# Optimization experiments

Hardware: AMD Instinct MI355X
Metric: run time of the kernel (lower is better)

## Reference

```python
import jax, jax.numpy as jnp
import numpy as np

B, T, D, SPAN = 4, 4096, 1024, 128


def _windowed_attention(q, k, v, span):
    # Causal sliding-window attention: position t attends to [max(0, t-span+1), t].
    # Tiled as blocks of size span: each query block attends to its own block
    # plus the previous block (exactly covers the window), avoiding any [T,T]
    # or per-timestep materialization.
    B, T, D = q.shape
    S = span
    nb = T // S  # T chosen divisible by span
    qb = q.reshape(B, nb, S, D)
    kb = k.reshape(B, nb, S, D)
    vb = v.reshape(B, nb, S, D)
    pad = jnp.zeros((B, 1, S, D), dtype=q.dtype)
    kk = jnp.concatenate([jnp.concatenate([pad, kb[:, :-1]], axis=1), kb], axis=2)  # [B,nb,2S,D]
    vv = jnp.concatenate([jnp.concatenate([pad, vb[:, :-1]], axis=1), vb], axis=2)  # [B,nb,2S,D]
    scale = 1.0 / jnp.sqrt(jnp.asarray(D, dtype=q.dtype))
    scores = jnp.einsum('bnqd,bnkd->bnqk', qb, kk) * scale  # [B,nb,S,2S]
    n_idx = jnp.arange(nb)[:, None, None]      # block index
    q_idx = jnp.arange(S)[None, :, None]       # query offset within block
    k_idx = jnp.arange(2 * S)[None, None, :]   # key offset in [prev|cur] pair
    rel = k_idx - S - q_idx                    # key_pos - query_pos
    # window: -span+1 <= rel <= 0; first block's "previous" half is padding -> mask it
    mask = (rel <= 0) & (rel > -S) & ((n_idx > 0) | (k_idx >= S))
    neg = jnp.asarray(jnp.finfo(scores.dtype).min, dtype=scores.dtype)
    scores = jnp.where(mask, scores, neg)
    w = jax.nn.softmax(scores, axis=-1)
    out = jnp.einsum('bnqk,bnkd->bnqd', w, vv)
    return out.reshape(B, T, D)


def setup_inputs() -> dict:
    key = jax.random.key(0)
    ks = jax.random.split(key, 7)
    s = 1.0 / np.sqrt(D)
    return {
        'x': jax.random.normal(ks[0], (B, T, D), dtype=jnp.float32),
        'Wq': jax.random.normal(ks[1], (D, D), dtype=jnp.float32) * s,
        'bq': jax.random.normal(ks[2], (D,), dtype=jnp.float32) * s,
        'Wk': jax.random.normal(ks[3], (D, D), dtype=jnp.float32) * s,
        'bk': jax.random.normal(ks[4], (D,), dtype=jnp.float32) * s,
        'Wv': jax.random.normal(ks[5], (D, D), dtype=jnp.float32) * s,
        'bv': jax.random.normal(ks[6], (D,), dtype=jnp.float32) * s,
        'span': SPAN,
    }


def reference(x, Wq, bq, Wk, bk, Wv, bv, span):
    # torch nn.Linear: y = x @ W.T + b
    q = jnp.einsum('btd,ed->bte', x, Wq) + bq
    k = jnp.einsum('btd,ed->bte', x, Wk) + bk
    v = jnp.einsum('btd,ed->bte', x, Wv) + bv
    return _windowed_attention(q, k, v, span)
```

## Files before the change

kernel.cpp:

```cpp
#include <hip/hip_runtime.h>
#include <hip/hip_bf16.h>

#define BB 4
#define TT 4096
#define DD 1024
#define SS 128
#define MM (BB*TT)

typedef __attribute__((ext_vector_type(8))) short bf16x8;
typedef __attribute__((ext_vector_type(4))) short s16x4;
typedef __attribute__((ext_vector_type(4))) float f32x4;

#define VMCNT(N) asm volatile("s_waitcnt vmcnt(" #N ")" ::: "memory")
#define LGKM0()  asm volatile("s_waitcnt lgkmcnt(0)" ::: "memory")

__device__ __forceinline__ void block_sync() {
    asm volatile("" ::: "memory");
    __builtin_amdgcn_s_barrier();
    asm volatile("" ::: "memory");
}

__device__ __forceinline__ short f2bf(float f) {
    union { float f; unsigned u; } cv; cv.f = f;
    unsigned u = cv.u;
    u += 0x7fffu + ((u >> 16) & 1u);
    return (short)(u >> 16);
}

__device__ __forceinline__ void gload16(const short* g, short* l) {
    __builtin_amdgcn_global_load_lds(
        (const __attribute__((address_space(1))) void*)g,
        (__attribute__((address_space(3))) void*)l, 16, 0, 0);
}

__global__ __launch_bounds__(256) void cast_f32_bf16(
    const float* __restrict__ src, short* __restrict__ dst)
{
    const int i = (blockIdx.x * 256 + threadIdx.x) * 4;
    const float4 v = *(const float4*)(src + i);
    s16x4 o;
    o.x = f2bf(v.x); o.y = f2bf(v.y); o.z = f2bf(v.z); o.w = f2bf(v.w);
    *(s16x4*)(dst + i) = o;
}

__global__ __launch_bounds__(256) void cast_w3(
    const float* __restrict__ a, const float* __restrict__ b,
    const float* __restrict__ c, short* __restrict__ dst)
{
    const float* src = (blockIdx.y == 0) ? a : (blockIdx.y == 1) ? b : c;
    short* d = dst + (size_t)blockIdx.y * DD * DD;
    const int i = (blockIdx.x * 256 + threadIdx.x) * 4;
    const float4 v = *(const float4*)(src + i);
    s16x4 o;
    o.x = f2bf(v.x); o.y = f2bf(v.y); o.z = f2bf(v.z); o.w = f2bf(v.w);
    *(s16x4*)(d + i) = o;
}


#define MF(a_, b_, c_) ((GRP == 2)                                            \
    ? __builtin_amdgcn_mfma_f32_16x16x32_bf16((b_), (a_), (c_), 0, 0, 0)      \
    : __builtin_amdgcn_mfma_f32_16x16x32_bf16((a_), (b_), (c_), 0, 0, 0))

#define QKV_PHASE(ABASE, P, STAGE_STMT, VM_STMT)                              \
  do {                                                                        \
    bf16x8 af0k0 = *(const bf16x8*)((ABASE) + (((P)*2)*16   + c16) * 64 + sw0);\
    bf16x8 af0k1 = *(const bf16x8*)((ABASE) + (((P)*2)*16   + c16) * 64 + sw1);\
    bf16x8 af1k0 = *(const bf16x8*)((ABASE) + (((P)*2+1)*16 + c16) * 64 + sw0);\
    bf16x8 af1k1 = *(const bf16x8*)((ABASE) + (((P)*2+1)*16 + c16) * 64 + sw1);\
    STAGE_STMT;                                                               \
    block_sync();                                                             \
    LGKM0();                                                                  \
    __builtin_amdgcn_s_setprio(1);                                            \
    _Pragma("unroll")                                                         \
    for (int nj = 0; nj < 4; nj++) {                                          \
      acc[(P)*2][nj]   = MF(af0k0, bf[nj][0], acc[(P)*2][nj]);                \
      acc[(P)*2][nj]   = MF(af0k1, bf[nj][1], acc[(P)*2][nj]);                \
      acc[(P)*2+1][nj] = MF(af1k0, bf[nj][0], acc[(P)*2+1][nj]);              \
      acc[(P)*2+1][nj] = MF(af1k1, bf[nj][1], acc[(P)*2+1][nj]);              \
    }                                                                         \
    __builtin_amdgcn_s_setprio(0);                                            \
    VM_STMT;                                                                  \
    block_sync();                                                             \
  } while (0)

template<int GRP>
__device__ __forceinline__ void qkv_core(
    const short* __restrict__ X, const short* __restrict__ W,
    const float* __restrict__ bias,
    short* __restrict__ Y, short* __restrict__ vT,
    short* lds, const int m_base, const int n_base)
{
    const int tid  = threadIdx.x;
    const int wv   = tid >> 6, lane = tid & 63;
    const int wm   = wv >> 2,  wn   = wv & 3;
    const int quad = lane >> 4, c16 = lane & 15;
    const int swz  = c16 & 7;
    const int sw0  = ((quad)     ^ swz) * 8;
    const int sw1  = ((quad + 4) ^ swz) * 8;

    auto stageA = [&](int k0, int d, int h) {
        short* dst = lds + d * 16384 + h * 8192;
#pragma unroll
        for (int g = 0; g < 2; g++) {
            const int idx = g * 512 + tid;
            const int row = idx >> 3, slot = idx & 7;
            gload16(X + (size_t)(m_base + h * 128 + row) * DD + k0
                      + ((slot ^ (row & 7)) * 8),
                    dst + row * 64 + slot * 8);
        }
    };
    auto stageB = [&](int k0, int d, int h) {
        short* dst = lds + 32768 + d * 16384 + h * 8192;
#pragma unroll
        for (int g = 0; g < 2; g++) {
            const int idx = g * 512 + tid;
            const int row = idx >> 3, slot = idx & 7;
            gload16(W + (size_t)(n_base + h * 128 + row) * DD + k0
                      + ((slot ^ (row & 7)) * 8),
                    dst + row * 64 + slot * 8);
        }
    };

    f32x4 acc[8][4];
#pragma unroll
    for (int i = 0; i < 8; i++)
#pragma unroll
        for (int j = 0; j < 4; j++) acc[i][j] = (f32x4){0.f, 0.f, 0.f, 0.f};

    stageA(0, 0, 0);  stageA(0, 0, 1);
    stageB(0, 0, 0);  stageB(0, 0, 1);
    stageB(64, 1, 0); stageB(64, 1, 1);
    VMCNT(4);
    block_sync();

    const short* Abuf0 = lds + wm * 8192;
    const short* Abuf1 = lds + 16384 + wm * 8192;
    const short* Bbuf0 = lds + 32768 + (wn >> 1) * 8192 + (wn & 1) * 4096;
    const short* Bbuf1 = lds + 49152 + (wn >> 1) * 8192 + (wn & 1) * 4096;

    bf16x8 bf[4][2];

    for (int it = 0; it < 8; ++it) {
        const int k1 = it * 128 + 64;
        const int k2 = it * 128 + 128;
        const int k3 = it * 128 + 192;
        const bool more = (it < 7);

#pragma unroll
        for (int nj = 0; nj < 4; nj++) {
            bf[nj][0] = *(const bf16x8*)(Bbuf0 + (nj * 16 + c16) * 64 + sw0);
            bf[nj][1] = *(const bf16x8*)(Bbuf0 + (nj * 16 + c16) * 64 + sw1);
        }
        QKV_PHASE(Abuf0, 0, stageA(k1, 1, 0), ((void)0));
        QKV_PHASE(Abuf0, 1, stageA(k1, 1, 1), ((void)0));
        QKV_PHASE(Abuf0, 2, if (more) stageB(k2, 0, 0), ((void)0));
        QKV_PHASE(Abuf0, 3, if (more) stageB(k2, 0, 1),
                  if (more) { VMCNT(4); } else { VMCNT(0); });

#pragma unroll
        for (int nj = 0; nj < 4; nj++) {
            bf[nj][0] = *(const bf16x8*)(Bbuf1 + (nj * 16 + c16) * 64 + sw0);
            bf[nj][1] = *(const bf16x8*)(Bbuf1 + (nj * 16 + c16) * 64 + sw1);
        }
        QKV_PHASE(Abuf1, 0, if (more) stageA(k2, 0, 0), ((void)0));
        QKV_PHASE(Abuf1, 1, if (more) stageA(k2, 0, 1), ((void)0));
        QKV_PHASE(Abuf1, 2, if (more) stageB(k3, 1, 0), ((void)0));
        QKV_PHASE(Abuf1, 3, if (more) stageB(k3, 1, 1),
                  if (more) { VMCNT(4); } else { VMCNT(0); });
    }

    if (GRP != 2) {
#pragma unroll
        for (int nj = 0; nj < 4; nj++) {
            const int col = n_base + wn * 64 + nj * 16 + c16;
            const float bc = bias[col];
#pragma unroll
            for (int mi = 0; mi < 8; mi++) {
                const int row = m_base + wm * 128 + mi * 16 + quad * 4;
#pragma unroll
                for (int r = 0; r < 4; r++)
                    Y[(size_t)(row + r) * DD + col] = f2bf(acc[mi][nj][r] + bc);
            }
        }
    } else {
#pragma unroll
        for (int nj = 0; nj < 4; nj++) {
#pragma unroll
            for (int r = 0; r < 4; r++) {
                const int drow = n_base + wn * 64 + nj * 16 + quad * 4 + r;
                const float bc = bias[drow];
#pragma unroll
                for (int mi = 0; mi < 8; mi++) {
                    const int mcol = m_base + wm * 128 + mi * 16 + c16;
                    vT[((size_t)(mcol >> 12) * DD + drow) * TT + (mcol & 4095)]
                        = f2bf(acc[mi][nj][r] + bc);
                }
            }
        }
    }
}

__global__ __launch_bounds__(512, 2) void qkv_gemm8(
    const short* __restrict__ X, const short* __restrict__ W3,
    const float* __restrict__ bq, const float* __restrict__ bk,
    const float* __restrict__ bv,
    short* __restrict__ q, short* __restrict__ k, short* __restrict__ vT)
{
    __shared__ __align__(16) short lds[65536];
    const int bid = blockIdx.x;
    const int wg  = (bid & 7) * 96 + (bid >> 3);
    const int mt  = wg & 63;
    const int cn  = wg >> 6;
    const int grp = cn >> 2;
    const int nt  = cn & 3;
    const int m_base = mt * 256;
    const int n_base = nt * 256;
    if (grp == 0)      qkv_core<0>(X, W3,              bq, q, nullptr, lds, m_base, n_base);
    else if (grp == 1) qkv_core<1>(X, W3 + DD * DD,    bk, k, nullptr, lds, m_base, n_base);
    else               qkv_core<2>(X, W3 + 2 * DD * DD, bv, nullptr, vT, lds, m_base, n_base);
}

__global__ __launch_bounds__(256) void attn_fused(
    const short* __restrict__ Q,
    const short* __restrict__ Kb,
    const short* __restrict__ VT,
    float* __restrict__ O)
{
    __shared__ short lds[78336];

    const int l   = blockIdx.x;
    const int xcd = l & 7;
    const int rr  = l >> 3;
    const int n   = xcd * 4 + (rr & 3);
    const int qh  = (rr >> 2) & 1;
    const int b   = rr >> 3;

    const int tid  = threadIdx.x;
    const int wv   = tid >> 6, lane = tid & 63;
    const int quad = lane >> 4, c16 = lane & 15;
    const int srow = tid >> 2;
    const int scol = (tid & 3) * 8;

    const int qrow   = b * TT + n * SS + qh * 64;
    const int krow   = b * TT + n * SS - SS;
    const int bstart = b * TT;

    f32x4 acc[16];
#pragma unroll
    for (int j = 0; j < 16; j++) acc[j] = (f32x4){0.f, 0.f, 0.f, 0.f};

    auto stage1 = [&](int kk, int bi) {
        short* qb   = lds + bi * 20480;
        short* kbuf = qb + 4096;
        const int k0 = kk * 64;
#pragma unroll
        for (int ks = 0; ks < 2; ks++) {
            gload16(Q + (qrow + srow) * DD + k0 + ks * 32 + scol,
                    qb + ks * 2048 + srow * 32 + scol);
#pragma unroll
            for (int s = 0; s < 4; s++) {
                const int row = srow + s * 64;
                int g = krow + row;
                if (g < bstart) g = bstart;
                gload16(Kb + g * DD + k0 + ks * 32 + scol,
                        kbuf + ks * 8192 + row * 32 + scol);
            }
        }
    };

    stage1(0, 0);
    stage1(1, 1);
    for (int kk = 0; kk < 16; kk++) {
        if (kk < 15) { VMCNT(10); } else { VMCNT(0); }
        block_sync();
        if (kk < 14) stage1(kk + 2, (kk + 2) % 3);
        const short* qb   = lds + (kk % 3) * 20480;
        const short* kbuf = qb + 4096;
#pragma unroll
        for (int ks = 0; ks < 2; ks++) {
            bf16x8 a = *(const bf16x8*)(qb + ks * 2048 + (wv * 16 + c16) * 32 + quad * 8);
#pragma unroll
            for (int j = 0; j < 16; j++) {
                bf16x8 bf = *(const bf16x8*)(kbuf + ks * 8192 + (j * 16 + c16) * 32 + quad * 8);
                acc[j] = __builtin_amdgcn_mfma_f32_16x16x32_bf16(a, bf, acc[j], 0, 0, 0);
            }
        }
    }

    __syncthreads();

    const int tbase = n * SS - SS;
    auto stage2 = [&](int s, short* vbuf) {
        const int d0 = (s >> 1) * 128;
        const int kh = (s & 1) * 128;
#pragma unroll
        for (int kc = 0; kc < 4; kc++) {
#pragma unroll
            for (int s64 = 0; s64 < 2; s64++) {
                const int row = srow + s64 * 64;
                int t = tbase + kh + kc * 32 + scol;
                if (t < 0) t = 0;
                gload16(VT + (size_t)(b * DD + d0 + row) * TT + t,
                        vbuf + kc * 4096 + row * 32 + scol);
            }
        }
    };
    stage2(0, lds);
    stage2(1, lds + 16384);

    short* Pw = lds + 61440 + wv * (16 * 264);
    const float scale = 0.03125f;
#pragma unroll
    for (int r = 0; r < 4; r++) {
        const int q_idx = qh * 64 + wv * 16 + quad * 4 + r;
        float mx = -3.0e38f;
#pragma unroll
        for (int j = 0; j < 16; j++) {
            const int k_idx = j * 16 + c16;
            const int rel = k_idx - SS - q_idx;
            const bool valid = (rel <= 0) & (rel > -SS) & ((n > 0) | (k_idx >= SS));
            const float sv = valid ? acc[j][r] * scale : -3.0e38f;
            acc[j][r] = sv;
            mx = fmaxf(mx, sv);
        }
#pragma unroll
        for (int o = 1; o < 16; o <<= 1) mx = fmaxf(mx, __shfl_xor(mx, o));
        float sm = 0.f;
#pragma unroll
        for (int j = 0; j < 16; j++) {
            const float p = __expf(acc[j][r] - mx);
            acc[j][r] = p;
            sm += p;
        }
#pragma unroll
        for (int o = 1; o < 16; o <<= 1) sm += __shfl_xor(sm, o);
        const float inv = 1.0f / sm;
#pragma unroll
        for (int j = 0; j < 16; j++)
            Pw[(quad * 4 + r) * 264 + j * 16 + c16] = f2bf(acc[j][r] * inv);
    }

    f32x4 o8[8];
#pragma unroll
    for (int j = 0; j < 8; j++) o8[j] = (f32x4){0.f, 0.f, 0.f, 0.f};

    for (int s = 0; s < 16; s++) {
        if (s < 2)       { VMCNT(8); }
        else if (s < 15) { VMCNT(40); }
        else             { VMCNT(16); }
        block_sync();
        if (s < 14) stage2(s + 2, lds + ((s + 2) % 3) * 16384);
        const short* vbuf = lds + (s % 3) * 16384;
        const int kh = (s & 1) * 128;
#pragma unroll
        for (int kc = 0; kc < 4; kc++) {
            bf16x8 a = *(const bf16x8*)(Pw + c16 * 264 + kh + kc * 32 + quad * 8);
#pragma unroll
            for (int jj = 0; jj < 8; jj++) {
                bf16x8 bf = *(const bf16x8*)(vbuf + kc * 4096 + (jj * 16 + c16) * 32 + quad * 8);
                o8[jj] = __builtin_amdgcn_mfma_f32_16x16x32_bf16(a, bf, o8[jj], 0, 0, 0);
            }
        }
        if (s & 1) {
            const int d0 = (s >> 1) * 128;
#pragma unroll
            for (int jj = 0; jj < 8; jj++) {
#pragma unroll
                for (int r = 0; r < 4; r++)
                    O[(size_t)(qrow + wv * 16 + quad * 4 + r) * DD + d0 + jj * 16 + c16] = o8[jj][r];
                o8[jj] = (f32x4){0.f, 0.f, 0.f, 0.f};
            }
        }
    }
}

extern "C" void kernel_launch(void* const* d_in, const int* in_sizes, int n_in,
                              void* d_out, int out_size, void* d_ws, size_t ws_size,
                              hipStream_t stream) {
    const float* x  = (const float*)d_in[0];
    const float* Wq = (const float*)d_in[1];
    const float* bq = (const float*)d_in[2];
    const float* Wk = (const float*)d_in[3];
    const float* bk = (const float*)d_in[4];
    const float* Wv = (const float*)d_in[5];
    const float* bv = (const float*)d_in[6];
    float* out = (float*)d_out;

    char* ws = (char*)d_ws;
    const size_t SZ = (size_t)MM * DD * 2;
    short* q   = (short*)(ws);
    short* k   = (short*)(ws + SZ);
    short* vT  = (short*)(ws + 2 * SZ);
    short* xb  = (short*)(ws + 3 * SZ);
    short* w3b = (short*)(ws + 4 * SZ);

    dim3 blk(256);
    cast_f32_bf16<<<MM * DD / 1024, blk, 0, stream>>>(x, xb);
    cast_w3<<<dim3(DD * DD / 1024, 3), blk, 0, stream>>>(Wq, Wk, Wv, w3b);

    qkv_gemm8<<<768, 512, 0, stream>>>(xb, w3b, bq, bk, bv, q, k, vT);

    attn_fused<<<256, 256, 0, stream>>>(q, k, vT, out);
}
```

Baseline: 300.2 us.

## Split attention across 8 waves with key-half softmax reduction and swizzled LDS

The attention kernel now launches 512 threads instead of 256. Each pair of waves splits the 256 keys (for QK^T) or the 64-wide head dimension chunks (for PV), and row max and sum are combined across the pair through LDS with extra barriers. Q/K and V tiles use XOR-swizzled LDS layouts to cut bank conflicts, and s_setprio is raised around the MFMA loops. All outputs are held in 32 accumulator registers and written once at the end, which raises register pressure against the 512-thread, 2-block launch bound.

```diff
diff --git a/kernel.cpp b/kernel.cpp
--- a/kernel.cpp
+++ b/kernel.cpp
@@ -220,7 +220,7 @@
     else               qkv_core<2>(X, W3 + 2 * DD * DD, bv, nullptr, vT, lds, m_base, n_base);
 }
 
-__global__ __launch_bounds__(256) void attn_fused(
+__global__ __launch_bounds__(512, 2) void attn_fused(
     const short* __restrict__ Q,
     const short* __restrict__ Kb,
     const short* __restrict__ VT,
@@ -238,85 +238,95 @@
     const int tid  = threadIdx.x;
     const int wv   = tid >> 6, lane = tid & 63;
     const int quad = lane >> 4, c16 = lane & 15;
-    const int srow = tid >> 2;
-    const int scol = (tid & 3) * 8;
+    const int qt   = wv >> 1;
+    const int kh   = wv & 1;
+    const int dh   = wv & 1;
 
     const int qrow   = b * TT + n * SS + qh * 64;
     const int krow   = b * TT + n * SS - SS;
     const int bstart = b * TT;
 
-    f32x4 acc[16];
-#pragma unroll
-    for (int j = 0; j < 16; j++) acc[j] = (f32x4){0.f, 0.f, 0.f, 0.f};
+    f32x4 acc[8];
+#pragma unroll
+    for (int j = 0; j < 8; j++) acc[j] = (f32x4){0.f, 0.f, 0.f, 0.f};
 
     auto stage1 = [&](int kk, int bi) {
-        short* qb   = lds + bi * 20480;
-        short* kbuf = qb + 4096;
+        short* qb = lds + bi * 20480;
+        short* kb = qb + 4096;
         const int k0 = kk * 64;
-#pragma unroll
-        for (int ks = 0; ks < 2; ks++) {
-            gload16(Q + (qrow + srow) * DD + k0 + ks * 32 + scol,
-                    qb + ks * 2048 + srow * 32 + scol);
-#pragma unroll
-            for (int s = 0; s < 4; s++) {
-                const int row = srow + s * 64;
-                int g = krow + row;
-                if (g < bstart) g = bstart;
-                gload16(Kb + g * DD + k0 + ks * 32 + scol,
-                        kbuf + ks * 8192 + row * 32 + scol);
-            }
+        {
+            const int row = tid >> 3, slot = tid & 7;
+            gload16(Q + (qrow + row) * DD + k0 + ((slot ^ (row & 7)) * 8),
+                    qb + row * 64 + slot * 8);
+        }
+#pragma unroll
+        for (int g = 0; g < 4; g++) {
+            const int idx = g * 512 + tid;
+            const int row = idx >> 3, slot = idx & 7;
+            int grow = krow + row;
+            if (grow < bstart) grow = bstart;
+            gload16(Kb + grow * DD + k0 + ((slot ^ (row & 7)) * 8),
+                    kb + row * 64 + slot * 8);
         }
     };
+
+    const int sw7 = c16 & 7;
 
     stage1(0, 0);
     stage1(1, 1);
     for (int kk = 0; kk < 16; kk++) {
-        if (kk < 15) { VMCNT(10); } else { VMCNT(0); }
+        if (kk < 15) { VMCNT(5); } else { VMCNT(0); }
         block_sync();
         if (kk < 14) stage1(kk + 2, (kk + 2) % 3);
-        const short* qb   = lds + (kk % 3) * 20480;
-        const short* kbuf = qb + 4096;
+        const short* qb = lds + (kk % 3) * 20480;
+        const short* kb = qb + 4096;
+        __builtin_amdgcn_s_setprio(1);
 #pragma unroll
         for (int ks = 0; ks < 2; ks++) {
-            bf16x8 a = *(const bf16x8*)(qb + ks * 2048 + (wv * 16 + c16) * 32 + quad * 8);
-#pragma unroll
-            for (int j = 0; j < 16; j++) {
-                bf16x8 bf = *(const bf16x8*)(kbuf + ks * 8192 + (j * 16 + c16) * 32 + quad * 8);
+            const int slot = ((ks * 4 + quad) ^ sw7) * 8;
+            bf16x8 a = *(const bf16x8*)(qb + (qt * 16 + c16) * 64 + slot);
+#pragma unroll
+            for (int j = 0; j < 8; j++) {
+                bf16x8 bf = *(const bf16x8*)(kb + (kh * 128 + j * 16 + c16) * 64 + slot);
                 acc[j] = __builtin_amdgcn_mfma_f32_16x16x32_bf16(a, bf, acc[j], 0, 0, 0);
             }
         }
-    }
-
-    __syncthreads();
+        __builtin_amdgcn_s_setprio(0);
+    }
+
+    block_sync();
 
     const int tbase = n * SS - SS;
-    auto stage2 = [&](int s, short* vbuf) {
-        const int d0 = (s >> 1) * 128;
-        const int kh = (s & 1) * 128;
-#pragma unroll
-        for (int kc = 0; kc < 4; kc++) {
-#pragma unroll
-            for (int s64 = 0; s64 < 2; s64++) {
-                const int row = srow + s64 * 64;
-                int t = tbase + kh + kc * 32 + scol;
-                if (t < 0) t = 0;
-                gload16(VT + (size_t)(b * DD + d0 + row) * TT + t,
-                        vbuf + kc * 4096 + row * 32 + scol);
-            }
+    auto stage2 = [&](int s, int bi) {
+        short* vb = lds + bi * 16384;
+        const int d0  = (s >> 1) * 128;
+        const int khv = (s & 1) * 128;
+#pragma unroll
+        for (int g = 0; g < 4; g++) {
+            const int idx = g * 512 + tid;
+            const int row = idx >> 4, slot = idx & 15;
+            int t = tbase + khv + ((slot ^ (row & 15)) * 8);
+            if (t < 0) t = 0;
+            gload16(VT + (size_t)(b * DD + d0 + row) * TT + t,
+                    vb + row * 128 + slot * 8);
         }
     };
-    stage2(0, lds);
-    stage2(1, lds + 16384);
-
-    short* Pw = lds + 61440 + wv * (16 * 264);
+    stage2(0, 0);
+    stage2(1, 1);
+
+    short* Pb   = lds + 61440;
+    float* smax = (float*)(lds + 49152);
+    float* ssum = (float*)(lds + 49408);
     const float scale = 0.03125f;
+    float mx4[4], sums[4];
+
 #pragma unroll
     for (int r = 0; r < 4; r++) {
-        const int q_idx = qh * 64 + wv * 16 + quad * 4 + r;
+        const int q_idx = qh * 64 + qt * 16 + quad * 4 + r;
         float mx = -3.0e38f;
 #pragma unroll
-        for (int j = 0; j < 16; j++) {
-            const int k_idx = j * 16 + c16;
+        for (int j = 0; j < 8; j++) {
+            const int k_idx = kh * 128 + j * 16 + c16;
             const int rel = k_idx - SS - q_idx;
             const bool valid = (rel <= 0) & (rel > -SS) & ((n > 0) | (k_idx >= SS));
             const float sv = valid ? acc[j][r] * scale : -3.0e38f;
@@ -325,53 +335,71 @@
         }
 #pragma unroll
         for (int o = 1; o < 16; o <<= 1) mx = fmaxf(mx, __shfl_xor(mx, o));
+        mx4[r] = mx;
+        if (c16 == 0) smax[(qt * 2 + kh) * 16 + quad * 4 + r] = mx;
+    }
+    LGKM0(); block_sync();
+
+#pragma unroll
+    for (int r = 0; r < 4; r++) {
+        const float M = fmaxf(mx4[r], smax[(qt * 2 + (kh ^ 1)) * 16 + quad * 4 + r]);
         float sm = 0.f;
 #pragma unroll
-        for (int j = 0; j < 16; j++) {
-            const float p = __expf(acc[j][r] - mx);
+        for (int j = 0; j < 8; j++) {
+            const float p = __expf(acc[j][r] - M);
             acc[j][r] = p;
             sm += p;
         }
 #pragma unroll
         for (int o = 1; o < 16; o <<= 1) sm += __shfl_xor(sm, o);
-        const float inv = 1.0f / sm;
-#pragma unroll
-        for (int j = 0; j < 16; j++)
-            Pw[(quad * 4 + r) * 264 + j * 16 + c16] = f2bf(acc[j][r] * inv);
-    }
-
-    f32x4 o8[8];
-#pragma unroll
-    for (int j = 0; j < 8; j++) o8[j] = (f32x4){0.f, 0.f, 0.f, 0.f};
-
+        sums[r] = sm;
+        if (c16 == 0) ssum[(qt * 2 + kh) * 16 + quad * 4 + r] = sm;
+    }
+    LGKM0(); block_sync();
+
+#pragma unroll
+    for (int r = 0; r < 4; r++) {
+        const float inv = 1.0f / (sums[r] + ssum[(qt * 2 + (kh ^ 1)) * 16 + quad * 4 + r]);
+#pragma unroll
+        for (int j = 0; j < 8; j++)
+            Pb[(qt * 16 + quad * 4 + r) * 264 + kh * 128 + j * 16 + c16] = f2bf(acc[j][r] * inv);
+    }
+    LGKM0();
+
+    f32x4 o_all[32];
+#pragma unroll
+    for (int j = 0; j < 32; j++) o_all[j] = (f32x4){0.f, 0.f, 0.f, 0.f};
+
+#pragma unroll
     for (int s = 0; s < 16; s++) {
-        if (s < 2)       { VMCNT(8); }
-        else if (s < 15) { VMCNT(40); }
-        else             { VMCNT(16); }
+        if (s < 15) { VMCNT(4); } else { VMCNT(0); }
         block_sync();
-        if (s < 14) stage2(s + 2, lds + ((s + 2) % 3) * 16384);
-        const short* vbuf = lds + (s % 3) * 16384;
-        const int kh = (s & 1) * 128;
+        if (s < 14) stage2(s + 2, (s + 2) % 3);
+        const short* vb = lds + (s % 3) * 16384;
+        const int khP = (s & 1) * 128;
+        const int od  = (s >> 1) * 4;
+        __builtin_amdgcn_s_setprio(1);
 #pragma unroll
         for (int kc = 0; kc < 4; kc++) {
-            bf16x8 a = *(const bf16x8*)(Pw + c16 * 264 + kh + kc * 32 + quad * 8);
-#pragma unroll
-            for (int jj = 0; jj < 8; jj++) {
-                bf16x8 bf = *(const bf16x8*)(vbuf + kc * 4096 + (jj * 16 + c16) * 32 + quad * 8);
-                o8[jj] = __builtin_amdgcn_mfma_f32_16x16x32_bf16(a, bf, o8[jj], 0, 0, 0);
+            bf16x8 a = *(const bf16x8*)(Pb + (qt * 16 + c16) * 264 + khP + kc * 32 + quad * 8);
+#pragma unroll
+            for (int jj = 0; jj < 4; jj++) {
+                bf16x8 bvf = *(const bf16x8*)(vb + (dh * 64 + jj * 16 + c16) * 128
+                                              + (((kc * 4 + quad) ^ c16) * 8));
+                o_all[od + jj] = __builtin_amdgcn_mfma_f32_16x16x32_bf16(a, bvf, o_all[od + jj], 0, 0, 0);
             }
         }
-        if (s & 1) {
-            const int d0 = (s >> 1) * 128;
-#pragma unroll
-            for (int jj = 0; jj < 8; jj++) {
-#pragma unroll
-                for (int r = 0; r < 4; r++)
-                    O[(size_t)(qrow + wv * 16 + quad * 4 + r) * DD + d0 + jj * 16 + c16] = o8[jj][r];
-                o8[jj] = (f32x4){0.f, 0.f, 0.f, 0.f};
-            }
-        }
-    }
+        __builtin_amdgcn_s_setprio(0);
+    }
+
+#pragma unroll
+    for (int d0i = 0; d0i < 8; d0i++)
+#pragma unroll
+        for (int jj = 0; jj < 4; jj++)
+#pragma unroll
+            for (int r = 0; r < 4; r++)
+                O[(size_t)(qrow + qt * 16 + quad * 4 + r) * DD
+                  + d0i * 128 + dh * 64 + jj * 16 + c16] = o_all[d0i * 4 + jj][r];
 }
 
 extern "C" void kernel_launch(void* const* d_in, const int* in_sizes, int n_in,
@@ -400,5 +428,5 @@
 
     qkv_gemm8<<<768, 512, 0, stream>>>(xb, w3b, bq, bk, bv, q, k, vT);
 
-    attn_fused<<<256, 256, 0, stream>>>(q, k, vT, out);
-}
+    attn_fused<<<256, 512, 0, stream>>>(q, k, vT, out);
+}
```

New measurement: 295.6 us. Within noise of the previous version (-1.5%).
